# Kernel tuning notes

Hardware: AMD Instinct MI355X
Metric: run time of the kernel (lower is better)

Reference implementation:

```python
import jax, jax.numpy as jnp
import numpy as np

B, T, D = 64, 512, 1024
V_TAG, V_TYPE = 6, 20
TAG_PAD, TYPE_PAD = 5, 19
E = 2048          # total entity spans in the batch (sliced cascade mode)
MAX_SPAN = 8      # max entity span length


def setup_inputs() -> dict:
    key = jax.random.key(0)
    ks = jax.random.split(key, 12)
    full_hidden = jax.random.normal(ks[0], (B, T, D), dtype=jnp.float32)
    W_tag = jax.random.normal(ks[1], (D, V_TAG), dtype=jnp.float32) * 0.02
    b_tag = jnp.zeros((V_TAG,), jnp.float32)
    W_type = jax.random.normal(ks[2], (D, V_TYPE), dtype=jnp.float32) * 0.02
    b_type = jnp.zeros((V_TYPE,), jnp.float32)
    crf_start = jax.random.normal(ks[3], (V_TAG,), dtype=jnp.float32) * 0.1
    crf_end = jax.random.normal(ks[4], (V_TAG,), dtype=jnp.float32) * 0.1
    crf_trans = jax.random.normal(ks[5], (V_TAG, V_TAG), dtype=jnp.float32) * 0.1
    # ragged sequence lengths (>= MAX_SPAN+1 so all positions/spans are sane)
    seq_lens = jnp.maximum(jax.random.randint(ks[6], (B,), 1, T + 1), MAX_SPAN + 1).astype(jnp.int32)
    tag_ids = jax.random.randint(ks[7], (B, T), 0, V_TAG - 1).astype(jnp.int32)  # exclude pad tag
    ent_sample_ids = jax.random.randint(ks[8], (E,), 0, B).astype(jnp.int32)
    ent_starts = jax.random.randint(ks[9], (E,), 0, T - MAX_SPAN).astype(jnp.int32)
    ent_lens = jax.random.randint(ks[10], (E,), 1, MAX_SPAN + 1)
    ent_ends = (ent_starts + ent_lens).astype(jnp.int32)
    ent_type_ids = jax.random.randint(ks[11], (E,), 0, V_TYPE - 1).astype(jnp.int32)  # exclude pad type
    return dict(full_hidden=full_hidden, W_tag=W_tag, b_tag=b_tag, W_type=W_type,
                b_type=b_type, crf_start=crf_start, crf_end=crf_end, crf_trans=crf_trans,
                tag_ids=tag_ids, seq_lens=seq_lens, ent_sample_ids=ent_sample_ids,
                ent_starts=ent_starts, ent_ends=ent_ends, ent_type_ids=ent_type_ids)


def reference(full_hidden, W_tag, b_tag, W_type, b_type, crf_start, crf_end, crf_trans,
              tag_ids, seq_lens, ent_sample_ids, ent_starts, ent_ends, ent_type_ids):
    mask = jnp.arange(T)[None, :] < seq_lens[:, None]                  # [B,T] bool (tok_mask)
    maskf = mask.astype(full_hidden.dtype)

    # ---- base CRF decoder: tag projection + CRF NLL per sample ----
    tag_feats = full_hidden @ W_tag + b_tag                            # [B,T,V_TAG]

    # gold path score
    emit_scores = jnp.take_along_axis(tag_feats, tag_ids[..., None].astype(jnp.int32), axis=-1)[..., 0]  # [B,T]
    gold = crf_start[tag_ids[:, 0]] + jnp.sum(emit_scores * maskf, axis=1)
    trans_scores = crf_trans[tag_ids[:, :-1], tag_ids[:, 1:]]          # [B,T-1]
    gold = gold + jnp.sum(trans_scores * maskf[:, 1:], axis=1)
    last_tags = tag_ids[jnp.arange(B), seq_lens - 1]
    gold = gold + crf_end[last_tags]

    # log-partition via forward algorithm (log-sum-exp DP, lax.scan over time)
    alpha0 = crf_start[None, :] + tag_feats[:, 0]                      # [B,V]

    def step(alpha, xs):
        emit_t, mask_t = xs                                            # [B,V], [B]
        new = jax.scipy.special.logsumexp(
            alpha[:, :, None] + crf_trans[None, :, :] + emit_t[:, None, :], axis=1)
        return jnp.where(mask_t[:, None], new, alpha), None

    alphaT, _ = jax.lax.scan(step, alpha0,
                             (jnp.swapaxes(tag_feats, 0, 1)[1:], mask.T[1:]))
    logZ = jax.scipy.special.logsumexp(alphaT + crf_end[None, :], axis=-1)  # [B]
    tag_losses = logZ - gold                                           # per-sample CRF NLL

    # ---- sliced cascade: entity-span mean pooling + CE(sum) per sample ----
    type_feats = full_hidden @ W_type + b_type                         # [B,T,V_TYPE]
    csum = jnp.pad(jnp.cumsum(type_feats, axis=1), ((0, 0), (1, 0), (0, 0)))  # [B,T+1,V_TYPE]
    span_sum = csum[ent_sample_ids, ent_ends] - csum[ent_sample_ids, ent_starts]  # [E,V_TYPE]
    span_len = (ent_ends - ent_starts).astype(type_feats.dtype)
    ent_feats = span_sum / span_len[:, None]                           # mean over span
    logp = jax.nn.log_softmax(ent_feats, axis=-1)
    ent_ce = -jnp.take_along_axis(logp, ent_type_ids[:, None].astype(jnp.int32), axis=-1)[:, 0]
    valid = (ent_type_ids != TYPE_PAD).astype(ent_ce.dtype)            # ignore_index
    type_losses = jax.ops.segment_sum(ent_ce * valid, ent_sample_ids, num_segments=B)
    return tag_losses + type_losses                                    # [B]
```

## Files before the change

kernel.cpp:

```cpp
#include <hip/hip_runtime.h>
#include <math.h>
#include <stdint.h>

#define NB  64
#define NT  512
#define ND  1024
#define NVT 6
#define NVY 20
#define TYPE_PAD_V 19
#define NE  2048
#define LOG2E 1.44269504088896340736f
#define LN2   0.69314718055994530942f

typedef float v2f __attribute__((ext_vector_type(2)));

#define OFF_WTT 196608
#define OFF_CNT 217088
#define OFF_WS2 217104

__global__ __launch_bounds__(256) void k1_tagfeats(const float* __restrict__ H,
                                                   const float* __restrict__ W_tag,
                                                   const float* __restrict__ b_tag,
                                                   const float* __restrict__ W_type,
                                                   float* __restrict__ ws,
                                                   float* __restrict__ out) {
    float* featsT = ws;
    float* WtT    = ws + OFF_WTT;
    if (blockIdx.x == 0) {
        if (threadIdx.x < NB) out[threadIdx.x] = 0.0f;
        if (threadIdx.x == 64) ((int*)(ws + OFF_CNT))[0] = 0;
    }
    if (blockIdx.x < 32) {
        int tid = blockIdx.x * 256 + threadIdx.x;
        for (int i = tid; i < NVY * ND; i += 32 * 256)
            WtT[i] = W_type[(i & (ND - 1)) * NVY + (i >> 10)];
    }

    __shared__ float wlds[NVT][ND];
    for (int i = threadIdx.x; i < ND * NVT; i += 256) {
        int d = i / NVT, v = i % NVT;
        wlds[v][d] = W_tag[i];
    }
    __syncthreads();
    float bt[NVT];
#pragma unroll
    for (int v = 0; v < NVT; ++v) bt[v] = b_tag[v];

    const int lane = threadIdx.x & 63;
    const int wid  = threadIdx.x >> 6;
    const int qw   = lane >> 4;
    const int ql   = lane & 15;
    const int r0 = blockIdx.x * 64 + wid * 16 + qw * 4;
    const float* hp = H + (size_t)r0 * ND;

    float acc[4][NVT];
#pragma unroll
    for (int rr = 0; rr < 4; ++rr)
#pragma unroll
        for (int v = 0; v < NVT; ++v) acc[rr][v] = 0.0f;

#pragma unroll
    for (int k = 0; k < 16; ++k) {
        float4 ha = ((const float4*)hp)[ql + 16 * k];
        float4 hb = ((const float4*)(hp + ND))[ql + 16 * k];
        float4 hc = ((const float4*)(hp + 2 * ND))[ql + 16 * k];
        float4 hd = ((const float4*)(hp + 3 * ND))[ql + 16 * k];
#pragma unroll
        for (int v = 0; v < NVT; ++v) {
            float4 w = ((const float4*)&wlds[v][0])[ql + 16 * k];
            acc[0][v] = __builtin_fmaf(ha.x, w.x, acc[0][v]);
            acc[0][v] = __builtin_fmaf(ha.y, w.y, acc[0][v]);
            acc[0][v] = __builtin_fmaf(ha.z, w.z, acc[0][v]);
            acc[0][v] = __builtin_fmaf(ha.w, w.w, acc[0][v]);
            acc[1][v] = __builtin_fmaf(hb.x, w.x, acc[1][v]);
            acc[1][v] = __builtin_fmaf(hb.y, w.y, acc[1][v]);
            acc[1][v] = __builtin_fmaf(hb.z, w.z, acc[1][v]);
            acc[1][v] = __builtin_fmaf(hb.w, w.w, acc[1][v]);
            acc[2][v] = __builtin_fmaf(hc.x, w.x, acc[2][v]);
            acc[2][v] = __builtin_fmaf(hc.y, w.y, acc[2][v]);
            acc[2][v] = __builtin_fmaf(hc.z, w.z, acc[2][v]);
            acc[2][v] = __builtin_fmaf(hc.w, w.w, acc[2][v]);
            acc[3][v] = __builtin_fmaf(hd.x, w.x, acc[3][v]);
            acc[3][v] = __builtin_fmaf(hd.y, w.y, acc[3][v]);
            acc[3][v] = __builtin_fmaf(hd.z, w.z, acc[3][v]);
            acc[3][v] = __builtin_fmaf(hd.w, w.w, acc[3][v]);
        }
    }
#pragma unroll
    for (int rr = 0; rr < 4; ++rr)
#pragma unroll
        for (int v = 0; v < NVT; ++v) {
#pragma unroll
            for (int off = 8; off >= 1; off >>= 1)
                acc[rr][v] += __shfl_xor(acc[rr][v], off);
        }
    const int bb = r0 >> 9;
#pragma unroll
    for (int rr = 0; rr < 4; ++rr) {
        const int tt = (r0 + rr) & (NT - 1);
        float val = acc[rr][0] + bt[0];
        val = (ql == 1) ? acc[rr][1] + bt[1] : val;
        val = (ql == 2) ? acc[rr][2] + bt[2] : val;
        val = (ql == 3) ? acc[rr][3] + bt[3] : val;
        val = (ql == 4) ? acc[rr][4] + bt[4] : val;
        val = (ql == 5) ? acc[rr][5] + bt[5] : val;
        if (ql < 6)
            featsT[(size_t)tt * 384 + bb * 6 + ql] = val;
    }
}

#define LOADC(BUF, c) do {                                                   \
    _Pragma("unroll")                                                        \
    for (int kk = 0; kk < 6; ++kk) {                                         \
        const float4* p = src4 + (size_t)((c) * 6 + kk) * 128;               \
        BUF[2 * kk] = p[0]; BUF[2 * kk + 1] = p[1];                          \
    }                                                                        \
} while (0)

#define CBODY(BUF, c) do {                                                   \
    float i0 = BUF[1].z, i1 = BUF[3].z, i2 = BUF[5].z,                       \
          i3 = BUF[7].z, i4 = BUF[9].z, i5 = BUF[11].z;                      \
    float im = fmaxf(fmaxf(fmaxf(i0, i1), i2), fmaxf(fmaxf(i3, i4), i5));    \
    float w0 = q0 * __builtin_amdgcn_exp2f(i0 - im);                         \
    float w1 = q1 * __builtin_amdgcn_exp2f(i1 - im);                         \
    float w2 = q2 * __builtin_amdgcn_exp2f(i2 - im);                         \
    float w3 = q3 * __builtin_amdgcn_exp2f(i3 - im);                         \
    float w4 = q4 * __builtin_amdgcn_exp2f(i4 - im);                         \
    float w5 = q5 * __builtin_amdgcn_exp2f(i5 - im);                         \
    float n0 = BUF[0].x * w0, n1 = BUF[0].y * w0, n2 = BUF[0].z * w0,        \
          n3 = BUF[0].w * w0, n4 = BUF[1].x * w0, n5 = BUF[1].y * w0;        \
    n0 = __builtin_fmaf(BUF[2].x,  w1, n0); n1 = __builtin_fmaf(BUF[2].y,  w1, n1); \
    n2 = __builtin_fmaf(BUF[2].z,  w1, n2); n3 = __builtin_fmaf(BUF[2].w,  w1, n3); \
    n4 = __builtin_fmaf(BUF[3].x,  w1, n4); n5 = __builtin_fmaf(BUF[3].y,  w1, n5); \
    n0 = __builtin_fmaf(BUF[4].x,  w2, n0); n1 = __builtin_fmaf(BUF[4].y,  w2, n1); \
    n2 = __builtin_fmaf(BUF[4].z,  w2, n2); n3 = __builtin_fmaf(BUF[4].w,  w2, n3); \
    n4 = __builtin_fmaf(BUF[5].x,  w2, n4); n5 = __builtin_fmaf(BUF[5].y,  w2, n5); \
    n0 = __builtin_fmaf(BUF[6].x,  w3, n0); n1 = __builtin_fmaf(BUF[6].y,  w3, n1); \
    n2 = __builtin_fmaf(BUF[6].z,  w3, n2); n3 = __builtin_fmaf(BUF[6].w,  w3, n3); \
    n4 = __builtin_fmaf(BUF[7].x,  w3, n4); n5 = __builtin_fmaf(BUF[7].y,  w3, n5); \
    n0 = __builtin_fmaf(BUF[8].x,  w4, n0); n1 = __builtin_fmaf(BUF[8].y,  w4, n1); \
    n2 = __builtin_fmaf(BUF[8].z,  w4, n2); n3 = __builtin_fmaf(BUF[8].w,  w4, n3); \
    n4 = __builtin_fmaf(BUF[9].x,  w4, n4); n5 = __builtin_fmaf(BUF[9].y,  w4, n5); \
    n0 = __builtin_fmaf(BUF[10].x, w5, n0); n1 = __builtin_fmaf(BUF[10].y, w5, n1); \
    n2 = __builtin_fmaf(BUF[10].z, w5, n2); n3 = __builtin_fmaf(BUF[10].w, w5, n3); \
    n4 = __builtin_fmaf(BUF[11].x, w5, n4); n5 = __builtin_fmaf(BUF[11].y, w5, n5); \
    float qmax = fmaxf(fmaxf(fmaxf(n0, n1), n2), fmaxf(fmaxf(n3, n4), n5));  \
    uint32_t eb = __float_as_uint(qmax) >> 23;                               \
    mAcc2 += (float)((int)eb - 126) + im;                                    \
    float ri = __uint_as_float((uint32_t)(253 - eb) << 23);                  \
    q0 = n0 * ri; q1 = n1 * ri; q2 = n2 * ri;                                \
    q3 = n3 * ri; q4 = n4 * ri; q5 = n5 * ri;                                \
    int lc = (c) + 3; if (lc > 31) lc = 31;                                  \
    LOADC(BUF, lc);                                                          \
} while (0)

__global__ __launch_bounds__(64) void k2_fused(
    const float* __restrict__ H,
    const float* __restrict__ b_type,
    const float* __restrict__ crf_start,
    const float* __restrict__ crf_end,
    const float* __restrict__ crf_trans,
    const int* __restrict__ tag_ids,
    const int* __restrict__ seq_lens,
    const int* __restrict__ ent_sid,
    const int* __restrict__ ent_st,
    const int* __restrict__ ent_en,
    const int* __restrict__ ent_ty,
    float* __restrict__ ws,
    float* __restrict__ out) {
    const float* featsT = ws;
    const float* WtT    = ws + OFF_WTT;
    int* cnt            = (int*)(ws + OFF_CNT);
    float* ws2          = ws + OFF_WS2;
    __shared__ int stag[NT];
    __shared__ float trLp[NVT * NVT];
    __shared__ int isLast;
    const int lane = threadIdx.x;

    if (blockIdx.x < 192) {
        const int c = blockIdx.x / 6;
        const int k = blockIdx.x - 6 * c;
        const int b = lane;
        const int L = seq_lens[b];
        float F[NVT][NVT];
#pragma unroll
        for (int i = 0; i < NVT; ++i)
#pragma unroll
            for (int j = 0; j < NVT; ++j)
                F[i][j] = __builtin_amdgcn_exp2f(crf_trans[i * NVT + j] * LOG2E);
        const char* pf = (const char*)featsT + b * 24;
        v2f Ebuf[16][3];
#pragma unroll
        for (int u = 0; u < 16; ++u) {
            const v2f* p = (const v2f*)(pf + (size_t)(16 * c + 1 + u) * 1536);
            Ebuf[u][0] = p[0]; Ebuf[u][1] = p[1]; Ebuf[u][2] = p[2];
        }
        float v0, v1, v2, v3, v4, v5;
        v0 = (k == 0) ? 1.f : 0.f; v1 = (k == 1) ? 1.f : 0.f; v2 = (k == 2) ? 1.f : 0.f;
        v3 = (k == 3) ? 1.f : 0.f; v4 = (k == 4) ? 1.f : 0.f; v5 = (k == 5) ? 1.f : 0.f;
        int isc = 0;
#pragma unroll
        for (int u = 0; u < 16; ++u) {
            float e0 = __builtin_amdgcn_exp2f(Ebuf[u][0].x * LOG2E);
            float e1 = __builtin_amdgcn_exp2f(Ebuf[u][0].y * LOG2E);
            float e2 = __builtin_amdgcn_exp2f(Ebuf[u][1].x * LOG2E);
            float e3 = __builtin_amdgcn_exp2f(Ebuf[u][1].y * LOG2E);
            float e4 = __builtin_amdgcn_exp2f(Ebuf[u][2].x * LOG2E);
            float e5 = __builtin_amdgcn_exp2f(Ebuf[u][2].y * LOG2E);
            bool ok = (16 * c + 1 + u) < L;
            float g[NVT];
#pragma unroll
            for (int j = 0; j < NVT; ++j) {
                float s = F[0][j] * v0;
                s = __builtin_fmaf(F[1][j], v1, s);
                s = __builtin_fmaf(F[2][j], v2, s);
                s = __builtin_fmaf(F[3][j], v3, s);
                s = __builtin_fmaf(F[4][j], v4, s);
                s = __builtin_fmaf(F[5][j], v5, s);
                g[j] = s;
            }
            v0 = ok ? e0 * g[0] : v0;  v1 = ok ? e1 * g[1] : v1;
            v2 = ok ? e2 * g[2] : v2;  v3 = ok ? e3 * g[3] : v3;
            v4 = ok ? e4 * g[4] : v4;  v5 = ok ? e5 * g[5] : v5;
            if ((u & 3) == 3) {
                float qmax = fmaxf(fmaxf(fmaxf(v0, v1), v2), fmaxf(fmaxf(v3, v4), v5));
                uint32_t eb = __float_as_uint(qmax) >> 23;
                float ri = __uint_as_float((uint32_t)(253 - eb) << 23);
                v0 *= ri; v1 *= ri; v2 *= ri; v3 *= ri; v4 *= ri; v5 *= ri;
                isc += (int)eb - 126;
            }
        }
        float4* dst = (float4*)(ws2 + (((size_t)c * 6 + k) * 64 + b) * 8);
        dst[0] = make_float4(v0, v1, v2, v3);
        dst[1] = make_float4(v4, v5, (float)isc, 0.0f);

        __threadfence();
        if (lane == 0) isLast = (atomicAdd(cnt, 1) == 191);
        __syncthreads();
        if (isLast) {
            __threadfence();
            const int b2 = lane;
            float a0[NVT];
#pragma unroll
            for (int j = 0; j < NVT; ++j) a0[j] = crf_start[j] + featsT[b2 * 6 + j];
            float m0 = fmaxf(fmaxf(fmaxf(a0[0], a0[1]), a0[2]),
                             fmaxf(fmaxf(a0[3], a0[4]), a0[5]));
            float q0 = __builtin_amdgcn_exp2f((a0[0] - m0) * LOG2E);
            float q1 = __builtin_amdgcn_exp2f((a0[1] - m0) * LOG2E);
            float q2 = __builtin_amdgcn_exp2f((a0[2] - m0) * LOG2E);
            float q3 = __builtin_amdgcn_exp2f((a0[3] - m0) * LOG2E);
            float q4 = __builtin_amdgcn_exp2f((a0[4] - m0) * LOG2E);
            float q5 = __builtin_amdgcn_exp2f((a0[5] - m0) * LOG2E);
            float mAcc2 = m0 * LOG2E;

            const float4* src4 = (const float4*)ws2 + b2 * 2;
            float4 PB0[12], PB1[12], PB2[12];
            LOADC(PB0, 0); LOADC(PB1, 1); LOADC(PB2, 2);
#pragma unroll 1
            for (int c0 = 0; c0 < 30; c0 += 3) {
                CBODY(PB0, c0);
                CBODY(PB1, c0 + 1);
                CBODY(PB2, c0 + 2);
            }
            CBODY(PB0, 30);
            CBODY(PB1, 31);

            float zs = q0 * __builtin_amdgcn_exp2f(crf_end[0] * LOG2E)
                     + q1 * __builtin_amdgcn_exp2f(crf_end[1] * LOG2E)
                     + q2 * __builtin_amdgcn_exp2f(crf_end[2] * LOG2E)
                     + q3 * __builtin_amdgcn_exp2f(crf_end[3] * LOG2E)
                     + q4 * __builtin_amdgcn_exp2f(crf_end[4] * LOG2E)
                     + q5 * __builtin_amdgcn_exp2f(crf_end[5] * LOG2E);
            float logZ = LN2 * (mAcc2 + __builtin_amdgcn_logf(zs));
            atomicAdd(&out[b2], logZ);
        }
    } else if (blockIdx.x < 192 + NB) {
        const int b = blockIdx.x - 192;
        for (int i = lane; i < NT; i += 64) stag[i] = tag_ids[b * NT + i];
        if (lane < NVT * NVT) trLp[lane] = crf_trans[lane];
        __syncthreads();
        const int L = seq_lens[b];
        float g = 0.0f;
#pragma unroll
        for (int k = 0; k < NT / 64; ++k) {
            int t = lane + 64 * k;
            if (t < L) {
                int tg = stag[t];
                g += featsT[(size_t)t * 384 + b * 6 + tg];
                if (t >= 1) g += trLp[stag[t - 1] * NVT + tg];
            }
        }
#pragma unroll
        for (int off = 32; off >= 1; off >>= 1) g += __shfl_xor(g, off);
        if (lane == 0)
            atomicAdd(&out[b], -(g + crf_start[stag[0]] + crf_end[stag[L - 1]]));
    } else {
        const int e  = blockIdx.x - 192 - NB;
        const int bb = ent_sid[e];
        const int s  = ent_st[e];
        const int en = ent_en[e];
        const int ty = ent_ty[e];
        float4 sv[4];
#pragma unroll
        for (int k = 0; k < 4; ++k) { sv[k].x = 0.f; sv[k].y = 0.f; sv[k].z = 0.f; sv[k].w = 0.f; }
        for (int t = s; t < en; ++t) {
            const float4* hr = (const float4*)(H + ((size_t)bb * NT + t) * ND);
#pragma unroll
            for (int k = 0; k < 4; ++k) {
                float4 h = hr[lane + 64 * k];
                sv[k].x += h.x; sv[k].y += h.y; sv[k].z += h.z; sv[k].w += h.w;
            }
        }
        const float inv = 1.0f / (float)(en - s);
        float f[NVY];
#pragma unroll
        for (int v = 0; v < NVY; ++v) {
            const float4* wv = (const float4*)(WtT + v * ND);
            float p = 0.0f;
#pragma unroll
            for (int k = 0; k < 4; ++k) {
                float4 w = wv[lane + 64 * k];
                p += sv[k].x * w.x + sv[k].y * w.y + sv[k].z * w.z + sv[k].w * w.w;
            }
#pragma unroll
            for (int off = 32; off >= 1; off >>= 1) p += __shfl_xor(p, off);
            f[v] = p * inv + b_type[v];
        }
        float mx = -3.0e38f;
#pragma unroll
        for (int v = 0; v < NVY; ++v) mx = fmaxf(mx, f[v]);
        float sum = 0.0f, goldf = 0.0f;
#pragma unroll
        for (int v = 0; v < NVY; ++v) {
            sum += __expf(f[v] - mx);
            if (v == ty) goldf = f[v];
        }
        float lse = mx + __logf(sum);
        if (ty != TYPE_PAD_V && lane == 0) atomicAdd(&out[bb], lse - goldf);
    }
}

extern "C" void kernel_launch(void* const* d_in, const int* in_sizes, int n_in,
                              void* d_out, int out_size, void* d_ws, size_t ws_size,
                              hipStream_t stream) {
    const float* H         = (const float*)d_in[0];
    const float* W_tag     = (const float*)d_in[1];
    const float* b_tag     = (const float*)d_in[2];
    const float* W_type    = (const float*)d_in[3];
    const float* b_type    = (const float*)d_in[4];
    const float* crf_start = (const float*)d_in[5];
    const float* crf_end   = (const float*)d_in[6];
    const float* crf_trans = (const float*)d_in[7];
    const int* tag_ids     = (const int*)d_in[8];
    const int* seq_lens    = (const int*)d_in[9];
    const int* ent_sid     = (const int*)d_in[10];
    const int* ent_st      = (const int*)d_in[11];
    const int* ent_en      = (const int*)d_in[12];
    const int* ent_ty      = (const int*)d_in[13];
    float* out = (float*)d_out;
    float* ws  = (float*)d_ws;

    hipLaunchKernelGGL(k1_tagfeats, dim3(512), dim3(256), 0, stream,
                       H, W_tag, b_tag, W_type, ws, out);
    hipLaunchKernelGGL(k2_fused, dim3(192 + NB + NE), dim3(64), 0, stream,
                       H, b_type, crf_start, crf_end, crf_trans,
                       tag_ids, seq_lens, ent_sid, ent_st, ent_en, ent_ty, ws, out);
}
```

Baseline: 61.93 us.

## Split CRF chunk combine into separate kernel, shrink chunk register buffers

Removes the atomic-counter last-block pattern: the CRF cross-chunk combine now runs in a new single-block third kernel instead of inside whichever chunk block finishes last. The chunk blocks now load feature rows in groups of four rather than buffering all 16 timesteps at once, and the kernel gets a launch_bounds occupancy hint of 4. The entity path batches all 20 wave reductions after the dot products instead of reducing each one separately. The intent is lower register pressure and fewer serialized fences, at the cost of an extra kernel launch and less memory-level parallelism per chunk block.

```diff
diff --git a/kernel.cpp b/kernel.cpp
--- a/kernel.cpp
+++ b/kernel.cpp
@@ -15,7 +15,6 @@
 typedef float v2f __attribute__((ext_vector_type(2)));
 
 #define OFF_WTT 196608
-#define OFF_CNT 217088
 #define OFF_WS2 217104
 
 __global__ __launch_bounds__(256) void k1_tagfeats(const float* __restrict__ H,
@@ -26,10 +25,7 @@
                                                    float* __restrict__ out) {
     float* featsT = ws;
     float* WtT    = ws + OFF_WTT;
-    if (blockIdx.x == 0) {
-        if (threadIdx.x < NB) out[threadIdx.x] = 0.0f;
-        if (threadIdx.x == 64) ((int*)(ws + OFF_CNT))[0] = 0;
-    }
+    if (blockIdx.x == 0 && threadIdx.x < NB) out[threadIdx.x] = 0.0f;
     if (blockIdx.x < 32) {
         int tid = blockIdx.x * 256 + threadIdx.x;
         for (int i = tid; i < NVY * ND; i += 32 * 256)
@@ -106,6 +102,156 @@
         val = (ql == 5) ? acc[rr][5] + bt[5] : val;
         if (ql < 6)
             featsT[(size_t)tt * 384 + bb * 6 + ql] = val;
+    }
+}
+
+__global__ __launch_bounds__(64, 4) void k2_fused(
+    const float* __restrict__ H,
+    const float* __restrict__ b_type,
+    const float* __restrict__ crf_start,
+    const float* __restrict__ crf_end,
+    const float* __restrict__ crf_trans,
+    const int* __restrict__ tag_ids,
+    const int* __restrict__ seq_lens,
+    const int* __restrict__ ent_sid,
+    const int* __restrict__ ent_st,
+    const int* __restrict__ ent_en,
+    const int* __restrict__ ent_ty,
+    float* __restrict__ ws,
+    float* __restrict__ out) {
+    const float* featsT = ws;
+    const float* WtT    = ws + OFF_WTT;
+    float* ws2          = ws + OFF_WS2;
+    __shared__ int stag[NT];
+    __shared__ float trLp[NVT * NVT];
+    const int lane = threadIdx.x;
+
+    if (blockIdx.x < 192) {
+        const int c = blockIdx.x / 6;
+        const int k = blockIdx.x - 6 * c;
+        const int b = lane;
+        const int L = seq_lens[b];
+        float F[NVT][NVT];
+#pragma unroll
+        for (int i = 0; i < NVT; ++i)
+#pragma unroll
+            for (int j = 0; j < NVT; ++j)
+                F[i][j] = __builtin_amdgcn_exp2f(crf_trans[i * NVT + j] * LOG2E);
+        const char* pf = (const char*)featsT + b * 24;
+        float v0, v1, v2, v3, v4, v5;
+        v0 = (k == 0) ? 1.f : 0.f; v1 = (k == 1) ? 1.f : 0.f; v2 = (k == 2) ? 1.f : 0.f;
+        v3 = (k == 3) ? 1.f : 0.f; v4 = (k == 4) ? 1.f : 0.f; v5 = (k == 5) ? 1.f : 0.f;
+        int isc = 0;
+#pragma unroll 1
+        for (int grp = 0; grp < 4; ++grp) {
+            v2f Eb[4][3];
+#pragma unroll
+            for (int u = 0; u < 4; ++u) {
+                const v2f* p = (const v2f*)(pf + (size_t)(16 * c + 1 + 4 * grp + u) * 1536);
+                Eb[u][0] = p[0]; Eb[u][1] = p[1]; Eb[u][2] = p[2];
+            }
+#pragma unroll
+            for (int u = 0; u < 4; ++u) {
+                float e0 = __builtin_amdgcn_exp2f(Eb[u][0].x * LOG2E);
+                float e1 = __builtin_amdgcn_exp2f(Eb[u][0].y * LOG2E);
+                float e2 = __builtin_amdgcn_exp2f(Eb[u][1].x * LOG2E);
+                float e3 = __builtin_amdgcn_exp2f(Eb[u][1].y * LOG2E);
+                float e4 = __builtin_amdgcn_exp2f(Eb[u][2].x * LOG2E);
+                float e5 = __builtin_amdgcn_exp2f(Eb[u][2].y * LOG2E);
+                bool ok = (16 * c + 1 + 4 * grp + u) < L;
+                float g[NVT];
+#pragma unroll
+                for (int j = 0; j < NVT; ++j) {
+                    float s = F[0][j] * v0;
+                    s = __builtin_fmaf(F[1][j], v1, s);
+                    s = __builtin_fmaf(F[2][j], v2, s);
+                    s = __builtin_fmaf(F[3][j], v3, s);
+                    s = __builtin_fmaf(F[4][j], v4, s);
+                    s = __builtin_fmaf(F[5][j], v5, s);
+                    g[j] = s;
+                }
+                v0 = ok ? e0 * g[0] : v0;  v1 = ok ? e1 * g[1] : v1;
+                v2 = ok ? e2 * g[2] : v2;  v3 = ok ? e3 * g[3] : v3;
+                v4 = ok ? e4 * g[4] : v4;  v5 = ok ? e5 * g[5] : v5;
+            }
+            float qmax = fmaxf(fmaxf(fmaxf(v0, v1), v2), fmaxf(fmaxf(v3, v4), v5));
+            uint32_t eb = __float_as_uint(qmax) >> 23;
+            float ri = __uint_as_float((uint32_t)(253 - eb) << 23);
+            v0 *= ri; v1 *= ri; v2 *= ri; v3 *= ri; v4 *= ri; v5 *= ri;
+            isc += (int)eb - 126;
+        }
+        float4* dst = (float4*)(ws2 + (((size_t)c * 6 + k) * 64 + b) * 8);
+        dst[0] = make_float4(v0, v1, v2, v3);
+        dst[1] = make_float4(v4, v5, (float)isc, 0.0f);
+    } else if (blockIdx.x < 192 + NB) {
+        const int b = blockIdx.x - 192;
+        for (int i = lane; i < NT; i += 64) stag[i] = tag_ids[b * NT + i];
+        if (lane < NVT * NVT) trLp[lane] = crf_trans[lane];
+        __syncthreads();
+        const int L = seq_lens[b];
+        float g = 0.0f;
+#pragma unroll
+        for (int k = 0; k < NT / 64; ++k) {
+            int t = lane + 64 * k;
+            if (t < L) {
+                int tg = stag[t];
+                g += featsT[(size_t)t * 384 + b * 6 + tg];
+                if (t >= 1) g += trLp[stag[t - 1] * NVT + tg];
+            }
+        }
+#pragma unroll
+        for (int off = 32; off >= 1; off >>= 1) g += __shfl_xor(g, off);
+        if (lane == 0)
+            atomicAdd(&out[b], -(g + crf_start[stag[0]] + crf_end[stag[L - 1]]));
+    } else {
+        const int e  = blockIdx.x - 192 - NB;
+        const int bb = ent_sid[e];
+        const int s  = ent_st[e];
+        const int en = ent_en[e];
+        const int ty = ent_ty[e];
+        float4 sv[4];
+#pragma unroll
+        for (int k = 0; k < 4; ++k) { sv[k].x = 0.f; sv[k].y = 0.f; sv[k].z = 0.f; sv[k].w = 0.f; }
+        for (int t = s; t < en; ++t) {
+            const float4* hr = (const float4*)(H + ((size_t)bb * NT + t) * ND);
+#pragma unroll
+            for (int k = 0; k < 4; ++k) {
+                float4 h = hr[lane + 64 * k];
+                sv[k].x += h.x; sv[k].y += h.y; sv[k].z += h.z; sv[k].w += h.w;
+            }
+        }
+        const float inv = 1.0f / (float)(en - s);
+        float f[NVY];
+#pragma unroll
+        for (int v = 0; v < NVY; ++v) {
+            const float4* wv = (const float4*)(WtT + v * ND);
+            float p = 0.0f;
+#pragma unroll
+            for (int k = 0; k < 4; ++k) {
+                float4 w = wv[lane + 64 * k];
+                p += sv[k].x * w.x + sv[k].y * w.y + sv[k].z * w.z + sv[k].w * w.w;
+            }
+            f[v] = p;
+        }
+#pragma unroll
+        for (int off = 32; off >= 1; off >>= 1) {
+#pragma unroll
+            for (int v = 0; v < NVY; ++v) f[v] += __shfl_xor(f[v], off);
+        }
+        float mx = -3.0e38f;
+#pragma unroll
+        for (int v = 0; v < NVY; ++v) {
+            f[v] = f[v] * inv + b_type[v];
+            mx = fmaxf(mx, f[v]);
+        }
+        float sum = 0.0f, goldf = 0.0f;
+#pragma unroll
+        for (int v = 0; v < NVY; ++v) {
+            sum += __expf(f[v] - mx);
+            if (v == ty) goldf = f[v];
+        }
+        float lse = mx + __logf(sum);
+        if (ty != TYPE_PAD_V && lane == 0) atomicAdd(&out[bb], lse - goldf);
     }
 }
 
@@ -154,190 +300,47 @@
     LOADC(BUF, lc);                                                          \
 } while (0)
 
-__global__ __launch_bounds__(64) void k2_fused(
-    const float* __restrict__ H,
-    const float* __restrict__ b_type,
+__global__ __launch_bounds__(64) void k3_combine(
     const float* __restrict__ crf_start,
     const float* __restrict__ crf_end,
-    const float* __restrict__ crf_trans,
-    const int* __restrict__ tag_ids,
-    const int* __restrict__ seq_lens,
-    const int* __restrict__ ent_sid,
-    const int* __restrict__ ent_st,
-    const int* __restrict__ ent_en,
-    const int* __restrict__ ent_ty,
-    float* __restrict__ ws,
+    const float* __restrict__ ws,
     float* __restrict__ out) {
     const float* featsT = ws;
-    const float* WtT    = ws + OFF_WTT;
-    int* cnt            = (int*)(ws + OFF_CNT);
-    float* ws2          = ws + OFF_WS2;
-    __shared__ int stag[NT];
-    __shared__ float trLp[NVT * NVT];
-    __shared__ int isLast;
-    const int lane = threadIdx.x;
-
-    if (blockIdx.x < 192) {
-        const int c = blockIdx.x / 6;
-        const int k = blockIdx.x - 6 * c;
-        const int b = lane;
-        const int L = seq_lens[b];
-        float F[NVT][NVT];
-#pragma unroll
-        for (int i = 0; i < NVT; ++i)
-#pragma unroll
-            for (int j = 0; j < NVT; ++j)
-                F[i][j] = __builtin_amdgcn_exp2f(crf_trans[i * NVT + j] * LOG2E);
-        const char* pf = (const char*)featsT + b * 24;
-        v2f Ebuf[16][3];
-#pragma unroll
-        for (int u = 0; u < 16; ++u) {
-            const v2f* p = (const v2f*)(pf + (size_t)(16 * c + 1 + u) * 1536);
-            Ebuf[u][0] = p[0]; Ebuf[u][1] = p[1]; Ebuf[u][2] = p[2];
-        }
-        float v0, v1, v2, v3, v4, v5;
-        v0 = (k == 0) ? 1.f : 0.f; v1 = (k == 1) ? 1.f : 0.f; v2 = (k == 2) ? 1.f : 0.f;
-        v3 = (k == 3) ? 1.f : 0.f; v4 = (k == 4) ? 1.f : 0.f; v5 = (k == 5) ? 1.f : 0.f;
-        int isc = 0;
-#pragma unroll
-        for (int u = 0; u < 16; ++u) {
-            float e0 = __builtin_amdgcn_exp2f(Ebuf[u][0].x * LOG2E);
-            float e1 = __builtin_amdgcn_exp2f(Ebuf[u][0].y * LOG2E);
-            float e2 = __builtin_amdgcn_exp2f(Ebuf[u][1].x * LOG2E);
-            float e3 = __builtin_amdgcn_exp2f(Ebuf[u][1].y * LOG2E);
-            float e4 = __builtin_amdgcn_exp2f(Ebuf[u][2].x * LOG2E);
-            float e5 = __builtin_amdgcn_exp2f(Ebuf[u][2].y * LOG2E);
-            bool ok = (16 * c + 1 + u) < L;
-            float g[NVT];
-#pragma unroll
-            for (int j = 0; j < NVT; ++j) {
-                float s = F[0][j] * v0;
-                s = __builtin_fmaf(F[1][j], v1, s);
-                s = __builtin_fmaf(F[2][j], v2, s);
-                s = __builtin_fmaf(F[3][j], v3, s);
-                s = __builtin_fmaf(F[4][j], v4, s);
-                s = __builtin_fmaf(F[5][j], v5, s);
-                g[j] = s;
-            }
-            v0 = ok ? e0 * g[0] : v0;  v1 = ok ? e1 * g[1] : v1;
-            v2 = ok ? e2 * g[2] : v2;  v3 = ok ? e3 * g[3] : v3;
-            v4 = ok ? e4 * g[4] : v4;  v5 = ok ? e5 * g[5] : v5;
-            if ((u & 3) == 3) {
-                float qmax = fmaxf(fmaxf(fmaxf(v0, v1), v2), fmaxf(fmaxf(v3, v4), v5));
-                uint32_t eb = __float_as_uint(qmax) >> 23;
-                float ri = __uint_as_float((uint32_t)(253 - eb) << 23);
-                v0 *= ri; v1 *= ri; v2 *= ri; v3 *= ri; v4 *= ri; v5 *= ri;
-                isc += (int)eb - 126;
-            }
-        }
-        float4* dst = (float4*)(ws2 + (((size_t)c * 6 + k) * 64 + b) * 8);
-        dst[0] = make_float4(v0, v1, v2, v3);
-        dst[1] = make_float4(v4, v5, (float)isc, 0.0f);
-
-        __threadfence();
-        if (lane == 0) isLast = (atomicAdd(cnt, 1) == 191);
-        __syncthreads();
-        if (isLast) {
-            __threadfence();
-            const int b2 = lane;
-            float a0[NVT];
-#pragma unroll
-            for (int j = 0; j < NVT; ++j) a0[j] = crf_start[j] + featsT[b2 * 6 + j];
-            float m0 = fmaxf(fmaxf(fmaxf(a0[0], a0[1]), a0[2]),
-                             fmaxf(fmaxf(a0[3], a0[4]), a0[5]));
-            float q0 = __builtin_amdgcn_exp2f((a0[0] - m0) * LOG2E);
-            float q1 = __builtin_amdgcn_exp2f((a0[1] - m0) * LOG2E);
-            float q2 = __builtin_amdgcn_exp2f((a0[2] - m0) * LOG2E);
-            float q3 = __builtin_amdgcn_exp2f((a0[3] - m0) * LOG2E);
-            float q4 = __builtin_amdgcn_exp2f((a0[4] - m0) * LOG2E);
-            float q5 = __builtin_amdgcn_exp2f((a0[5] - m0) * LOG2E);
-            float mAcc2 = m0 * LOG2E;
-
-            const float4* src4 = (const float4*)ws2 + b2 * 2;
-            float4 PB0[12], PB1[12], PB2[12];
-            LOADC(PB0, 0); LOADC(PB1, 1); LOADC(PB2, 2);
+    const float* ws2    = ws + OFF_WS2;
+    const int b2 = threadIdx.x;
+    float a0[NVT];
+#pragma unroll
+    for (int j = 0; j < NVT; ++j) a0[j] = crf_start[j] + featsT[b2 * 6 + j];
+    float m0 = fmaxf(fmaxf(fmaxf(a0[0], a0[1]), a0[2]),
+                     fmaxf(fmaxf(a0[3], a0[4]), a0[5]));
+    float q0 = __builtin_amdgcn_exp2f((a0[0] - m0) * LOG2E);
+    float q1 = __builtin_amdgcn_exp2f((a0[1] - m0) * LOG2E);
+    float q2 = __builtin_amdgcn_exp2f((a0[2] - m0) * LOG2E);
+    float q3 = __builtin_amdgcn_exp2f((a0[3] - m0) * LOG2E);
+    float q4 = __builtin_amdgcn_exp2f((a0[4] - m0) * LOG2E);
+    float q5 = __builtin_amdgcn_exp2f((a0[5] - m0) * LOG2E);
+    float mAcc2 = m0 * LOG2E;
+
+    const float4* src4 = (const float4*)ws2 + b2 * 2;
+    float4 PB0[12], PB1[12], PB2[12];
+    LOADC(PB0, 0); LOADC(PB1, 1); LOADC(PB2, 2);
 #pragma unroll 1
-            for (int c0 = 0; c0 < 30; c0 += 3) {
-                CBODY(PB0, c0);
-                CBODY(PB1, c0 + 1);
-                CBODY(PB2, c0 + 2);
-            }
-            CBODY(PB0, 30);
-            CBODY(PB1, 31);
-
-            float zs = q0 * __builtin_amdgcn_exp2f(crf_end[0] * LOG2E)
-                     + q1 * __builtin_amdgcn_exp2f(crf_end[1] * LOG2E)
-                     + q2 * __builtin_amdgcn_exp2f(crf_end[2] * LOG2E)
-                     + q3 * __builtin_amdgcn_exp2f(crf_end[3] * LOG2E)
-                     + q4 * __builtin_amdgcn_exp2f(crf_end[4] * LOG2E)
-                     + q5 * __builtin_amdgcn_exp2f(crf_end[5] * LOG2E);
-            float logZ = LN2 * (mAcc2 + __builtin_amdgcn_logf(zs));
-            atomicAdd(&out[b2], logZ);
-        }
-    } else if (blockIdx.x < 192 + NB) {
-        const int b = blockIdx.x - 192;
-        for (int i = lane; i < NT; i += 64) stag[i] = tag_ids[b * NT + i];
-        if (lane < NVT * NVT) trLp[lane] = crf_trans[lane];
-        __syncthreads();
-        const int L = seq_lens[b];
-        float g = 0.0f;
-#pragma unroll
-        for (int k = 0; k < NT / 64; ++k) {
-            int t = lane + 64 * k;
-            if (t < L) {
-                int tg = stag[t];
-                g += featsT[(size_t)t * 384 + b * 6 + tg];
-                if (t >= 1) g += trLp[stag[t - 1] * NVT + tg];
-            }
-        }
-#pragma unroll
-        for (int off = 32; off >= 1; off >>= 1) g += __shfl_xor(g, off);
-        if (lane == 0)
-            atomicAdd(&out[b], -(g + crf_start[stag[0]] + crf_end[stag[L - 1]]));
-    } else {
-        const int e  = blockIdx.x - 192 - NB;
-        const int bb = ent_sid[e];
-        const int s  = ent_st[e];
-        const int en = ent_en[e];
-        const int ty = ent_ty[e];
-        float4 sv[4];
-#pragma unroll
-        for (int k = 0; k < 4; ++k) { sv[k].x = 0.f; sv[k].y = 0.f; sv[k].z = 0.f; sv[k].w = 0.f; }
-        for (int t = s; t < en; ++t) {
-            const float4* hr = (const float4*)(H + ((size_t)bb * NT + t) * ND);
-#pragma unroll
-            for (int k = 0; k < 4; ++k) {
-                float4 h = hr[lane + 64 * k];
-                sv[k].x += h.x; sv[k].y += h.y; sv[k].z += h.z; sv[k].w += h.w;
-            }
-        }
-        const float inv = 1.0f / (float)(en - s);
-        float f[NVY];
-#pragma unroll
-        for (int v = 0; v < NVY; ++v) {
-            const float4* wv = (const float4*)(WtT + v * ND);
-            float p = 0.0f;
-#pragma unroll
-            for (int k = 0; k < 4; ++k) {
-                float4 w = wv[lane + 64 * k];
-                p += sv[k].x * w.x + sv[k].y * w.y + sv[k].z * w.z + sv[k].w * w.w;
-            }
-#pragma unroll
-            for (int off = 32; off >= 1; off >>= 1) p += __shfl_xor(p, off);
-            f[v] = p * inv + b_type[v];
-        }
-        float mx = -3.0e38f;
-#pragma unroll
-        for (int v = 0; v < NVY; ++v) mx = fmaxf(mx, f[v]);
-        float sum = 0.0f, goldf = 0.0f;
-#pragma unroll
-        for (int v = 0; v < NVY; ++v) {
-            sum += __expf(f[v] - mx);
-            if (v == ty) goldf = f[v];
-        }
-        float lse = mx + __logf(sum);
-        if (ty != TYPE_PAD_V && lane == 0) atomicAdd(&out[bb], lse - goldf);
-    }
+    for (int c0 = 0; c0 < 30; c0 += 3) {
+        CBODY(PB0, c0);
+        CBODY(PB1, c0 + 1);
+        CBODY(PB2, c0 + 2);
+    }
+    CBODY(PB0, 30);
+    CBODY(PB1, 31);
+
+    float zs = q0 * __builtin_amdgcn_exp2f(crf_end[0] * LOG2E)
+             + q1 * __builtin_amdgcn_exp2f(crf_end[1] * LOG2E)
+             + q2 * __builtin_amdgcn_exp2f(crf_end[2] * LOG2E)
+             + q3 * __builtin_amdgcn_exp2f(crf_end[3] * LOG2E)
+             + q4 * __builtin_amdgcn_exp2f(crf_end[4] * LOG2E)
+             + q5 * __builtin_amdgcn_exp2f(crf_end[5] * LOG2E);
+    float logZ = LN2 * (mAcc2 + __builtin_amdgcn_logf(zs));
+    atomicAdd(&out[b2], logZ);
 }
 
 extern "C" void kernel_launch(void* const* d_in, const int* in_sizes, int n_in,
@@ -365,4 +368,6 @@
     hipLaunchKernelGGL(k2_fused, dim3(192 + NB + NE), dim3(64), 0, stream,
                        H, b_type, crf_start, crf_end, crf_trans,
                        tag_ids, seq_lens, ent_sid, ent_st, ent_en, ent_ty, ws, out);
+    hipLaunchKernelGGL(k3_combine, dim3(1), dim3(64), 0, stream,
+                       crf_start, crf_end, ws, out);
 }
```

New measurement: 71.59 us. +15.6%, slower.
